# Kernel tuning notes

Hardware: AMD Instinct MI355X
Metric: run time of the kernel (lower is better)

Reference implementation:

```python
import jax, jax.numpy as jnp
import numpy as np

N = 50000
D_IN, D_H1, D_H2 = 256, 128, 64
E = 1_600_000


def setup_inputs() -> dict:
    key = jax.random.key(0)
    k = jax.random.split(key, 6)
    x = jax.random.normal(k[0], (N, D_IN), dtype=jnp.float32)
    edge_index = jax.random.randint(k[1], (2, E), 0, N, dtype=jnp.int64)
    # Glorot-style init like torch_geometric GCNConv (weight [in, out], zero bias)
    W1 = jax.random.normal(k[2], (D_IN, D_H1), dtype=jnp.float32) * (2.0 / (D_IN + D_H1)) ** 0.5
    b1 = jnp.zeros((D_H1,), dtype=jnp.float32)
    W2 = jax.random.normal(k[3], (D_H1, D_H2), dtype=jnp.float32) * (2.0 / (D_H1 + D_H2)) ** 0.5
    b2 = jnp.zeros((D_H2,), dtype=jnp.float32)
    return {"x": x, "edge_index": edge_index, "W1": W1, "b1": b1, "W2": W2, "b2": b2}


def _gcn_norm(edge_index, n):
    # add self-loops, symmetric normalization: D^{-1/2} (A+I) D^{-1/2}
    loops = jnp.arange(n, dtype=edge_index.dtype)
    src = jnp.concatenate([edge_index[0], loops])
    dst = jnp.concatenate([edge_index[1], loops])
    deg = jnp.zeros((n,), jnp.float32).at[dst].add(1.0)
    dinv = jnp.where(deg > 0, jax.lax.rsqrt(deg), 0.0)
    w = dinv[src] * dinv[dst]  # [E+N]
    return src, dst, w


def _gcn_conv(x, W, b, src, dst, w, n):
    z = x @ W  # dense transform first (out_dim < in_dim)
    msg = z[src] * w[:, None]  # gather + scale, [E+N, out]
    out = jax.ops.segment_sum(msg, dst, num_segments=n)  # scatter-add
    return out + b


def reference(x, edge_index, W1, b1, W2, b2):
    src, dst, w = _gcn_norm(edge_index, N)
    z = jax.nn.relu(_gcn_conv(x, W1, b1, src, dst, w, N))
    z = jax.nn.relu(_gcn_conv(z, W2, b2, src, dst, w, N))
    return z
```

## Files before the change

### kernel.cpp

```cpp
#include <hip/hip_runtime.h>
#include <hip/hip_bf16.h>
#include <cstdint>
#include <cstddef>

#define NNODES 50000
#define NEDGES 1600000
#define DIN 256
#define DH1 128
#define DH2 64

#define NBKT 196
#define NCHUNK 128
#define CHUNKE 12500
#define STAGE_CAP 10240

__device__ __forceinline__ float bflo(uint32_t u) { return __uint_as_float(u << 16); }
__device__ __forceinline__ float bfhi(uint32_t u) { return __uint_as_float(u & 0xffff0000u); }
__device__ __forceinline__ uint16_t f2bf(float f) {
    uint32_t u = __float_as_uint(f);
    u += 0x7fffu + ((u >> 16) & 1u);
    return (uint16_t)(u >> 16);
}

__global__ __launch_bounds__(256) void k_chunkhist(const int* __restrict__ dst,
                                                   int* __restrict__ counts) {
    __shared__ int hist[NBKT];
    int c = blockIdx.x, t = threadIdx.x;
    if (t < NBKT) hist[t] = 0;
    __syncthreads();
    int e0 = c * CHUNKE, e1 = min(NEDGES, e0 + CHUNKE);
    for (int e = e0 + t; e < e1; e += 256) atomicAdd(&hist[dst[e] >> 8], 1);
    __syncthreads();
    if (t < NBKT) counts[c * NBKT + t] = hist[t];
}

__global__ __launch_bounds__(256) void k_bktscan(int* __restrict__ counts,
                                                 int* __restrict__ bktstart,
                                                 int* __restrict__ bktcnt) {
    __shared__ int lds[256];
    int t = threadIdx.x;
    int total = 0;
    if (t < NBKT)
        for (int c = 0; c < NCHUNK; ++c) total += counts[c * NBKT + t];
    lds[t] = total;
    __syncthreads();
    for (int d = 1; d < 256; d <<= 1) {
        int add = (t >= d) ? lds[t - d] : 0;
        __syncthreads();
        lds[t] += add;
        __syncthreads();
    }
    int base = lds[t] - total;
    if (t < NBKT) {
        bktstart[t] = base;
        bktcnt[t] = total;
        int run = base;
        for (int c = 0; c < NCHUNK; ++c) {
            int x = counts[c * NBKT + t];
            counts[c * NBKT + t] = run;
            run += x;
        }
    }
}

__global__ __launch_bounds__(256) void k_pairscatter(const int* __restrict__ src,
                                                     const int* __restrict__ dst,
                                                     const int* __restrict__ counts,
                                                     uint32_t* __restrict__ pairs) {
    __shared__ int cur[NBKT];
    int c = blockIdx.x, t = threadIdx.x;
    if (t < NBKT) cur[t] = counts[c * NBKT + t];
    __syncthreads();
    int e0 = c * CHUNKE, e1 = min(NEDGES, e0 + CHUNKE);
    for (int e = e0 + t; e < e1; e += 256) {
        int d = dst[e];
        int pos = atomicAdd(&cur[d >> 8], 1);
        pairs[pos] = ((uint32_t)(d & 255) << 16) | (uint32_t)src[e];
    }
}

__global__ __launch_bounds__(256) void k_sortbucket(const uint32_t* __restrict__ pairs,
                                                    const int* __restrict__ bktstart,
                                                    const int* __restrict__ bktcnt,
                                                    int* __restrict__ csr,
                                                    int* __restrict__ off,
                                                    float* __restrict__ dinv) {
    __shared__ int hist[256];
    __shared__ int cur[256];
    __shared__ int stage[STAGE_CAP];
    int b = blockIdx.x, t = threadIdx.x;
    int e0 = bktstart[b], ecnt = bktcnt[b];
    hist[t] = 0;
    __syncthreads();
    for (int e = e0 + t; e < e0 + ecnt; e += 256)
        atomicAdd(&hist[pairs[e] >> 16], 1);
    __syncthreads();
    int v = hist[t];
    cur[t] = v;
    __syncthreads();
    for (int d = 1; d < 256; d <<= 1) {
        int add = (t >= d) ? cur[t - d] : 0;
        __syncthreads();
        cur[t] += add;
        __syncthreads();
    }
    int excl = cur[t] - v;
    int node = (b << 8) + t;
    if (node < NNODES) {
        off[node] = e0 + excl;
        dinv[node] = rsqrtf((float)(v + 1));
    }
    if (b == NBKT - 1 && t == 0) off[NNODES] = NEDGES;
    __syncthreads();
    cur[t] = e0 + excl;
    __syncthreads();
    if (ecnt <= STAGE_CAP) {
        for (int e = e0 + t; e < e0 + ecnt; e += 256) {
            uint32_t p = pairs[e];
            int pos = atomicAdd(&cur[p >> 16], 1);
            stage[pos - e0] = (int)(p & 0xFFFF);
        }
        __syncthreads();
        for (int i = t; i < ecnt; i += 256) csr[e0 + i] = stage[i];
    } else {
        for (int e = e0 + t; e < e0 + ecnt; e += 256) {
            uint32_t p = pairs[e];
            int pos = atomicAdd(&cur[p >> 16], 1);
            csr[pos] = (int)(p & 0xFFFF);
        }
    }
}

template <int K, int NN>
__global__ __launch_bounds__(256) void k_gemm_scale(const float* __restrict__ X,
                                                    const float* __restrict__ W,
                                                    const float* __restrict__ dinv,
                                                    uint16_t* __restrict__ Z) {
    constexpr int BM = 64, BN = 64, BK = 16;
    __shared__ float As[BK][BM + 4];
    __shared__ float Bs[BK][BN + 4];
    int bm = blockIdx.x * BM;
    int bn = blockIdx.y * BN;
    int t = threadIdx.x;
    int tx = t & 15, ty = t >> 4;
    float acc[4][4] = {};
    for (int k0 = 0; k0 < K; k0 += BK) {
        {
            int row = t >> 2;
            int q = (t & 3) * 4;
            float4 a = make_float4(0.f, 0.f, 0.f, 0.f);
            int gr = bm + row;
            if (gr < NNODES)
                a = *reinterpret_cast<const float4*>(X + (size_t)gr * K + k0 + q);
            As[q + 0][row] = a.x;
            As[q + 1][row] = a.y;
            As[q + 2][row] = a.z;
            As[q + 3][row] = a.w;
        }
        {
            int kr = t >> 4;
            int nc = (t & 15) * 4;
            float4 bv = *reinterpret_cast<const float4*>(W + (size_t)(k0 + kr) * NN + bn + nc);
            *reinterpret_cast<float4*>(&Bs[kr][nc]) = bv;
        }
        __syncthreads();
#pragma unroll
        for (int k = 0; k < BK; ++k) {
            float4 av = *reinterpret_cast<const float4*>(&As[k][ty * 4]);
            float4 bv = *reinterpret_cast<const float4*>(&Bs[k][tx * 4]);
            float a[4] = {av.x, av.y, av.z, av.w};
            float bb[4] = {bv.x, bv.y, bv.z, bv.w};
#pragma unroll
            for (int i = 0; i < 4; ++i)
#pragma unroll
                for (int j = 0; j < 4; ++j) acc[i][j] = fmaf(a[i], bb[j], acc[i][j]);
        }
        __syncthreads();
    }
#pragma unroll
    for (int i = 0; i < 4; ++i) {
        int m = bm + ty * 4 + i;
        if (m >= NNODES) continue;
        float di = dinv[m];
        uint32_t p0 = (uint32_t)f2bf(acc[i][0] * di) | ((uint32_t)f2bf(acc[i][1] * di) << 16);
        uint32_t p1 = (uint32_t)f2bf(acc[i][2] * di) | ((uint32_t)f2bf(acc[i][3] * di) << 16);
        *reinterpret_cast<uint2*>(Z + (size_t)m * NN + bn + tx * 4) = make_uint2(p0, p1);
    }
}

template <int D>
__global__ __launch_bounds__(256) void k_agg_bf(const uint16_t* __restrict__ zs,
                                                const int* __restrict__ csr,
                                                const int* __restrict__ off,
                                                const float* __restrict__ dinv,
                                                const float* __restrict__ bias,
                                                float* __restrict__ out) {
    int wid = (blockIdx.x * 256 + threadIdx.x) >> 6;
    int lane = threadIdx.x & 63;
    if (wid >= NNODES) return;
    int start = off[wid];
    int c = off[wid + 1] - start;
    float di = dinv[wid];
    if constexpr (D == 128) {
        const uint32_t* Z = reinterpret_cast<const uint32_t*>(zs);
        uint32_t us = Z[(size_t)wid * 64 + lane];
        float ax = bflo(us), ay = bfhi(us);
        float bx = 0, by = 0, cx = 0, cy = 0, dx = 0, dy = 0;
        int j = 0;
        for (; j + 3 < c; j += 4) {
            int s0 = csr[start + j], s1 = csr[start + j + 1];
            int s2 = csr[start + j + 2], s3 = csr[start + j + 3];
            uint32_t u0 = Z[(size_t)s0 * 64 + lane];
            uint32_t u1 = Z[(size_t)s1 * 64 + lane];
            uint32_t u2 = Z[(size_t)s2 * 64 + lane];
            uint32_t u3 = Z[(size_t)s3 * 64 + lane];
            ax += bflo(u0); ay += bfhi(u0);
            bx += bflo(u1); by += bfhi(u1);
            cx += bflo(u2); cy += bfhi(u2);
            dx += bflo(u3); dy += bfhi(u3);
        }
        for (; j < c; ++j) {
            uint32_t u = Z[(size_t)csr[start + j] * 64 + lane];
            ax += bflo(u); ay += bfhi(u);
        }
        float sx = (ax + bx) + (cx + dx);
        float sy = (ay + by) + (cy + dy);
        float2 bv = *reinterpret_cast<const float2*>(bias + lane * 2);
        float2 o;
        o.x = fmaxf(fmaf(sx, di, bv.x), 0.f);
        o.y = fmaxf(fmaf(sy, di, bv.y), 0.f);
        *reinterpret_cast<float2*>(out + (size_t)wid * 128 + lane * 2) = o;
    } else {
        float a = __uint_as_float(((uint32_t)zs[(size_t)wid * 64 + lane]) << 16);
        float b = 0, cc = 0, d = 0;
        int j = 0;
        for (; j + 3 < c; j += 4) {
            int s0 = csr[start + j], s1 = csr[start + j + 1];
            int s2 = csr[start + j + 2], s3 = csr[start + j + 3];
            a += __uint_as_float(((uint32_t)zs[(size_t)s0 * 64 + lane]) << 16);
            b += __uint_as_float(((uint32_t)zs[(size_t)s1 * 64 + lane]) << 16);
            cc += __uint_as_float(((uint32_t)zs[(size_t)s2 * 64 + lane]) << 16);
            d += __uint_as_float(((uint32_t)zs[(size_t)s3 * 64 + lane]) << 16);
        }
        for (; j < c; ++j)
            a += __uint_as_float(((uint32_t)zs[(size_t)csr[start + j] * 64 + lane]) << 16);
        float s = (a + b) + (cc + d);
        float o = fmaxf(fmaf(s, di, bias[lane]), 0.f);
        out[(size_t)wid * 64 + lane] = o;
    }
}

extern "C" void kernel_launch(void* const* d_in, const int* in_sizes, int n_in,
                              void* d_out, int out_size, void* d_ws, size_t ws_size,
                              hipStream_t stream) {
    const float* x = (const float*)d_in[0];
    const int* ei = (const int*)d_in[1];
    const float* W1 = (const float*)d_in[2];
    const float* b1 = (const float*)d_in[3];
    const float* W2 = (const float*)d_in[4];
    const float* b2 = (const float*)d_in[5];
    float* out = (float*)d_out;

    char* ws = (char*)d_ws;
    int* counts = (int*)(ws + 0);
    int* bktstart = (int*)(ws + 101376);
    int* bktcnt = (int*)(ws + 102400);
    int* off = (int*)(ws + 103424);
    float* dinv = (float*)(ws + 303616);
    int* csr = (int*)(ws + 503808);
    uint16_t* zs1 = (uint16_t*)(ws + 6904832);
    float* h1 = (float*)(ws + 19705856);
    uint32_t* pairs = (uint32_t*)h1;
    uint16_t* zs2 = zs1;

    const int* esrc = ei;
    const int* edst = ei + NEDGES;

    k_chunkhist<<<NCHUNK, 256, 0, stream>>>(edst, counts);
    k_bktscan<<<1, 256, 0, stream>>>(counts, bktstart, bktcnt);
    k_pairscatter<<<NCHUNK, 256, 0, stream>>>(esrc, edst, counts, pairs);
    k_sortbucket<<<NBKT, 256, 0, stream>>>(pairs, bktstart, bktcnt, csr, off, dinv);

    dim3 g1((NNODES + 63) / 64, DH1 / 64);
    k_gemm_scale<DIN, DH1><<<g1, 256, 0, stream>>>(x, W1, dinv, zs1);
    k_agg_bf<DH1><<<NNODES / 4, 256, 0, stream>>>(zs1, csr, off, dinv, b1, h1);

    dim3 g2((NNODES + 63) / 64, DH2 / 64);
    k_gemm_scale<DH1, DH2><<<g2, 256, 0, stream>>>(h1, W2, dinv, zs2);
    k_agg_bf<DH2><<<NNODES / 4, 256, 0, stream>>>(zs2, csr, off, dinv, b2, out);
}
```

Before: 349.9 us.

## Replace FP32 SIMT GEMMs with split-bf16 MFMA GEMMs and pre-transposed weights

Both dense transforms move from a scalar FMA tiled GEMM to MFMA 16x16x32 bf16 instructions. Accuracy is kept close to fp32 by splitting each value into hi and lo bf16 parts and using three products. Two small kernels pre-split and transpose W1 and W2 into bf16 hi/lo buffers. Each block now covers all output columns with swizzled LDS tiles, so X is read only once. In exchange the code gains split-conversion work in the A load path and scalar 16-bit output stores, and uses more LDS per block.

Measured after the change: 316.8 us. 1.1x faster.

```diff
diff --git a/kernel.cpp b/kernel.cpp
--- a/kernel.cpp
+++ b/kernel.cpp
@@ -21,6 +21,9 @@
     u += 0x7fffu + ((u >> 16) & 1u);
     return (uint16_t)(u >> 16);
 }
+
+using b8 = __attribute__((ext_vector_type(8))) short;
+using f4x = __attribute__((ext_vector_type(4))) float;
 
 __global__ __launch_bounds__(256) void k_chunkhist(const int* __restrict__ dst,
                                                    int* __restrict__ counts) {
@@ -132,59 +135,136 @@
 }
 
 template <int K, int NN>
-__global__ __launch_bounds__(256) void k_gemm_scale(const float* __restrict__ X,
-                                                    const float* __restrict__ W,
-                                                    const float* __restrict__ dinv,
-                                                    uint16_t* __restrict__ Z) {
-    constexpr int BM = 64, BN = 64, BK = 16;
-    __shared__ float As[BK][BM + 4];
-    __shared__ float Bs[BK][BN + 4];
-    int bm = blockIdx.x * BM;
-    int bn = blockIdx.y * BN;
-    int t = threadIdx.x;
-    int tx = t & 15, ty = t >> 4;
-    float acc[4][4] = {};
+__global__ __launch_bounds__(256) void k_wsplit(const float* __restrict__ W,
+                                                uint16_t* __restrict__ Wth,
+                                                uint16_t* __restrict__ Wtl) {
+    int idx = blockIdx.x * 256 + threadIdx.x;
+    if (idx >= K * NN) return;
+    int k = idx / NN, n = idx % NN;
+    float f = W[idx];
+    uint16_t h = f2bf(f);
+    uint16_t l = f2bf(f - bflo((uint32_t)h));
+    Wth[n * K + k] = h;
+    Wtl[n * K + k] = l;
+}
+
+template <int K, int NN>
+__global__ __launch_bounds__(256) void k_gemm_mfma(const float* __restrict__ X,
+                                                   const uint16_t* __restrict__ Wth,
+                                                   const uint16_t* __restrict__ Wtl,
+                                                   const float* __restrict__ dinv,
+                                                   uint16_t* __restrict__ Z) {
+    constexpr int BM = 64, BK = 64;
+    constexpr int NW = NN / 64;
+    __shared__ uint16_t Ah[BM * BK], Al[BM * BK], Wh[NN * BK], Wl[NN * BK];
+    const int t = threadIdx.x;
+    const int wave = t >> 6, lane = t & 63;
+    const int bm = blockIdx.x * BM;
+    const int r16 = lane & 15, kg = lane >> 4;
+    const int n0 = wave * (NW * 16);
+    f4x acc[4][NW] = {};
+
     for (int k0 = 0; k0 < K; k0 += BK) {
         {
-            int row = t >> 2;
-            int q = (t & 3) * 4;
-            float4 a = make_float4(0.f, 0.f, 0.f, 0.f);
-            int gr = bm + row;
-            if (gr < NNODES)
-                a = *reinterpret_cast<const float4*>(X + (size_t)gr * K + k0 + q);
-            As[q + 0][row] = a.x;
-            As[q + 1][row] = a.y;
-            As[q + 2][row] = a.z;
-            As[q + 3][row] = a.w;
+            int row = t >> 2, kq = (t & 3) * 16;
+            const float* xp = X + (size_t)(bm + row) * K + k0 + kq;
+            bool ok = (bm + row) < NNODES;
+            float v[16];
+#pragma unroll
+            for (int u = 0; u < 4; ++u) {
+                float4 f = ok ? *reinterpret_cast<const float4*>(xp + u * 4)
+                              : make_float4(0.f, 0.f, 0.f, 0.f);
+                v[u * 4 + 0] = f.x; v[u * 4 + 1] = f.y;
+                v[u * 4 + 2] = f.z; v[u * 4 + 3] = f.w;
+            }
+            uint16_t hh[16], ll[16];
+#pragma unroll
+            for (int u = 0; u < 16; ++u) {
+                uint16_t h = f2bf(v[u]);
+                hh[u] = h;
+                ll[u] = f2bf(v[u] - bflo((uint32_t)h));
+            }
+#pragma unroll
+            for (int j = 0; j < 2; ++j) {
+                int s = (t & 3) * 2 + j;
+                int idx = (row * 8 + (s ^ (row & 7))) * 8;
+                const uint16_t* hp = hh + j * 8;
+                const uint16_t* lp = ll + j * 8;
+                uint4 ph, pl;
+                ph.x = hp[0] | ((uint32_t)hp[1] << 16);
+                ph.y = hp[2] | ((uint32_t)hp[3] << 16);
+                ph.z = hp[4] | ((uint32_t)hp[5] << 16);
+                ph.w = hp[6] | ((uint32_t)hp[7] << 16);
+                pl.x = lp[0] | ((uint32_t)lp[1] << 16);
+                pl.y = lp[2] | ((uint32_t)lp[3] << 16);
+                pl.z = lp[4] | ((uint32_t)lp[5] << 16);
+                pl.w = lp[6] | ((uint32_t)lp[7] << 16);
+                *reinterpret_cast<uint4*>(&Ah[idx]) = ph;
+                *reinterpret_cast<uint4*>(&Al[idx]) = pl;
+            }
         }
         {
-            int kr = t >> 4;
-            int nc = (t & 15) * 4;
-            float4 bv = *reinterpret_cast<const float4*>(W + (size_t)(k0 + kr) * NN + bn + nc);
-            *reinterpret_cast<float4*>(&Bs[kr][nc]) = bv;
-        }
-        __syncthreads();
-#pragma unroll
-        for (int k = 0; k < BK; ++k) {
-            float4 av = *reinterpret_cast<const float4*>(&As[k][ty * 4]);
-            float4 bv = *reinterpret_cast<const float4*>(&Bs[k][tx * 4]);
-            float a[4] = {av.x, av.y, av.z, av.w};
-            float bb[4] = {bv.x, bv.y, bv.z, bv.w};
-#pragma unroll
-            for (int i = 0; i < 4; ++i)
-#pragma unroll
-                for (int j = 0; j < 4; ++j) acc[i][j] = fmaf(a[i], bb[j], acc[i][j]);
-        }
-        __syncthreads();
-    }
-#pragma unroll
-    for (int i = 0; i < 4; ++i) {
-        int m = bm + ty * 4 + i;
-        if (m >= NNODES) continue;
-        float di = dinv[m];
-        uint32_t p0 = (uint32_t)f2bf(acc[i][0] * di) | ((uint32_t)f2bf(acc[i][1] * di) << 16);
-        uint32_t p1 = (uint32_t)f2bf(acc[i][2] * di) | ((uint32_t)f2bf(acc[i][3] * di) << 16);
-        *reinterpret_cast<uint2*>(Z + (size_t)m * NN + bn + tx * 4) = make_uint2(p0, p1);
+            constexpr int TPR = 256 / NN;
+            constexpr int SPT = 8 / TPR;
+            int n = t / TPR, q = t % TPR;
+#pragma unroll
+            for (int j = 0; j < SPT; ++j) {
+                int s = q * SPT + j;
+                uint4 vh = *reinterpret_cast<const uint4*>(&Wth[(size_t)n * K + k0 + s * 8]);
+                uint4 vl = *reinterpret_cast<const uint4*>(&Wtl[(size_t)n * K + k0 + s * 8]);
+                int idx = (n * 8 + (s ^ (n & 7))) * 8;
+                *reinterpret_cast<uint4*>(&Wh[idx]) = vh;
+                *reinterpret_cast<uint4*>(&Wl[idx]) = vl;
+            }
+        }
+        __syncthreads();
+#pragma unroll
+        for (int ks = 0; ks < 2; ++ks) {
+            int kslot = ks * 4 + kg;
+            b8 a_h[4], a_l[4];
+#pragma unroll
+            for (int mt = 0; mt < 4; ++mt) {
+                int row = mt * 16 + r16;
+                int idx = (row * 8 + (kslot ^ (row & 7))) * 8;
+                a_h[mt] = *reinterpret_cast<const b8*>(&Ah[idx]);
+                a_l[mt] = *reinterpret_cast<const b8*>(&Al[idx]);
+            }
+            b8 b_h[NW], b_l[NW];
+#pragma unroll
+            for (int nt = 0; nt < NW; ++nt) {
+                int n = n0 + nt * 16 + r16;
+                int idx = (n * 8 + (kslot ^ (n & 7))) * 8;
+                b_h[nt] = *reinterpret_cast<const b8*>(&Wh[idx]);
+                b_l[nt] = *reinterpret_cast<const b8*>(&Wl[idx]);
+            }
+#pragma unroll
+            for (int mt = 0; mt < 4; ++mt)
+#pragma unroll
+                for (int nt = 0; nt < NW; ++nt) {
+                    acc[mt][nt] = __builtin_amdgcn_mfma_f32_16x16x32_bf16(
+                        a_h[mt], b_h[nt], acc[mt][nt], 0, 0, 0);
+                    acc[mt][nt] = __builtin_amdgcn_mfma_f32_16x16x32_bf16(
+                        a_h[mt], b_l[nt], acc[mt][nt], 0, 0, 0);
+                    acc[mt][nt] = __builtin_amdgcn_mfma_f32_16x16x32_bf16(
+                        a_l[mt], b_h[nt], acc[mt][nt], 0, 0, 0);
+                }
+        }
+        __syncthreads();
+    }
+#pragma unroll
+    for (int mt = 0; mt < 4; ++mt) {
+#pragma unroll
+        for (int i = 0; i < 4; ++i) {
+            int m = bm + mt * 16 + kg * 4 + i;
+            if (m < NNODES) {
+                float di = dinv[m];
+#pragma unroll
+                for (int nt = 0; nt < NW; ++nt) {
+                    int n = n0 + nt * 16 + r16;
+                    Z[(size_t)m * NN + n] = f2bf(acc[mt][nt][i] * di);
+                }
+            }
+        }
     }
 }
 
@@ -269,23 +349,29 @@
     float* dinv = (float*)(ws + 303616);
     int* csr = (int*)(ws + 503808);
     uint16_t* zs1 = (uint16_t*)(ws + 6904832);
-    float* h1 = (float*)(ws + 19705856);
+    uint16_t* wt1h = (uint16_t*)(ws + 19705856);
+    uint16_t* wt1l = (uint16_t*)(ws + 19771392);
+    uint16_t* wt2h = (uint16_t*)(ws + 19836928);
+    uint16_t* wt2l = (uint16_t*)(ws + 19853312);
+    float* h1 = (float*)(ws + 19870720);
     uint32_t* pairs = (uint32_t*)h1;
     uint16_t* zs2 = zs1;
 
     const int* esrc = ei;
     const int* edst = ei + NEDGES;
+
+    k_wsplit<DIN, DH1><<<(DIN * DH1 + 255) / 256, 256, 0, stream>>>(W1, wt1h, wt1l);
+    k_wsplit<DH1, DH2><<<(DH1 * DH2 + 255) / 256, 256, 0, stream>>>(W2, wt2h, wt2l);
 
     k_chunkhist<<<NCHUNK, 256, 0, stream>>>(edst, counts);
     k_bktscan<<<1, 256, 0, stream>>>(counts, bktstart, bktcnt);
     k_pairscatter<<<NCHUNK, 256, 0, stream>>>(esrc, edst, counts, pairs);
     k_sortbucket<<<NBKT, 256, 0, stream>>>(pairs, bktstart, bktcnt, csr, off, dinv);
 
-    dim3 g1((NNODES + 63) / 64, DH1 / 64);
-    k_gemm_scale<DIN, DH1><<<g1, 256, 0, stream>>>(x, W1, dinv, zs1);
+    int gm = (NNODES + 63) / 64;
+    k_gemm_mfma<DIN, DH1><<<gm, 256, 0, stream>>>(x, wt1h, wt1l, dinv, zs1);
     k_agg_bf<DH1><<<NNODES / 4, 256, 0, stream>>>(zs1, csr, off, dinv, b1, h1);
 
-    dim3 g2((NNODES + 63) / 64, DH2 / 64);
-    k_gemm_scale<DH1, DH2><<<g2, 256, 0, stream>>>(h1, W2, dinv, zs2);
+    k_gemm_mfma<DH1, DH2><<<gm, 256, 0, stream>>>(h1, wt2h, wt2l, dinv, zs2);
     k_agg_bf<DH2><<<NNODES / 4, 256, 0, stream>>>(zs2, csr, off, dinv, b2, out);
 }
```
